# Optimization experiments

Measured on AMD Instinct MI355X. Metric: run time of the kernel, lower is better.

Reference implementation:

```python
import jax, jax.numpy as jnp
import numpy as np

D_MODEL = 768
NUM_HEADS = 12
HEAD_DIM = D_MODEL // NUM_HEADS
BATCH = 1
SEQ = 4096


def setup_inputs() -> dict:
    key = jax.random.key(0)
    ks = jax.random.split(key, 11)
    s = 0.02
    return {
        "q": jax.random.normal(ks[0], (BATCH, SEQ, D_MODEL), jnp.float32),
        "k": jax.random.normal(ks[1], (BATCH, SEQ, D_MODEL), jnp.float32),
        "v": jax.random.normal(ks[2], (BATCH, SEQ, D_MODEL), jnp.float32),
        "Wq": jax.random.normal(ks[3], (D_MODEL, D_MODEL), jnp.float32) * s,
        "bq": jnp.zeros((D_MODEL,), jnp.float32),
        "Wk": jax.random.normal(ks[4], (D_MODEL, D_MODEL), jnp.float32) * s,
        "bk": jnp.zeros((D_MODEL,), jnp.float32),
        "Wv": jax.random.normal(ks[5], (D_MODEL, D_MODEL), jnp.float32) * s,
        "bv": jnp.zeros((D_MODEL,), jnp.float32),
        "Wo": jax.random.normal(ks[6], (D_MODEL, D_MODEL), jnp.float32) * s,
        "bo": jnp.zeros((D_MODEL,), jnp.float32),
    }


def reference(q, k, v, Wq, bq, Wk, bk, Wv, bv, Wo, bo):
    B, S, D = q.shape
    H, Hd = NUM_HEADS, HEAD_DIM
    # linear projections (torch Linear: x @ W.T + b)
    qh = (q @ Wq.T + bq).reshape(B, S, H, Hd).transpose(0, 2, 1, 3)  # [B,H,S,Hd]
    kh = (k @ Wk.T + bk).reshape(B, S, H, Hd).transpose(0, 2, 1, 3)
    vh = (v @ Wv.T + bv).reshape(B, S, H, Hd).transpose(0, 2, 1, 3)
    scale = 1.0 / jnp.sqrt(jnp.asarray(Hd, qh.dtype))
    scores = jnp.einsum("bhsd,bhtd->bhst", qh, kh) * scale  # [B,H,S,S]
    weights = jax.nn.softmax(scores, axis=-1)
    attn = jnp.einsum("bhst,bhtd->bhsd", weights, vh)  # [B,H,S,Hd]
    attn = attn.transpose(0, 2, 1, 3).reshape(B, S, D)
    return attn @ Wo.T + bo
```

## Files before the change

### kernel.cpp

```cpp
#include <hip/hip_runtime.h>

#define S_LEN 4096
#define DMODEL 768
#define NHEAD 12
#define HD 64

typedef __bf16 bf16x8 __attribute__((ext_vector_type(8)));
typedef __bf16 bf16x4 __attribute__((ext_vector_type(4)));
typedef float f32x4 __attribute__((ext_vector_type(4)));
typedef float f32x16 __attribute__((ext_vector_type(16)));
typedef unsigned short u16x8 __attribute__((ext_vector_type(8)));
typedef unsigned short u16x4 __attribute__((ext_vector_type(4)));
typedef _Float16 f16x4 __attribute__((ext_vector_type(4)));

#if __has_builtin(__builtin_amdgcn_exp2f)
#define EXP2F(x) __builtin_amdgcn_exp2f(x)
#else
#define EXP2F(x) exp2f(x)
#endif

#define MFMA32(a, b, c) __builtin_amdgcn_mfma_f32_32x32x16_bf16(a, b, c, 0, 0, 0)

__device__ __forceinline__ unsigned short f2bf(float f) {
  unsigned int u = __float_as_uint(f);
  u += 0x7fffu + ((u >> 16) & 1u);
  return (unsigned short)(u >> 16);
}

__device__ __forceinline__ void gload_lds16(const void* g, void* l) {
  __builtin_amdgcn_global_load_lds(
      (__attribute__((address_space(1))) void*)g,
      (__attribute__((address_space(3))) void*)l, 16, 0, 0);
}

struct CvtArgs {
  const float* src[7];
  unsigned short* dst[7];
  int n[7];
};

__global__ __launch_bounds__(256) void cvt_kernel(CvtArgs a) {
  const int seg = blockIdx.y;
  const int n = a.n[seg];
  const int i = (blockIdx.x * 256 + threadIdx.x) * 8;
  if (i >= n) return;
  const float* s = a.src[seg] + i;
  u16x8 o;
#pragma unroll
  for (int j = 0; j < 8; ++j) o[j] = f2bf(s[j]);
  *reinterpret_cast<u16x8*>(a.dst[seg] + i) = o;
}

struct QkvArgs {
  const unsigned short* A[3];
  const unsigned short* W[3];
  const float* bias[3];
  unsigned short* dst[3];
  float scale[3];
};

__global__ __launch_bounds__(256) void qkv_gemm(QkvArgs a) {
  __shared__ unsigned char lds[32768];
  const int z = blockIdx.z;
  const unsigned short* __restrict__ A = a.A[z];
  const unsigned short* __restrict__ B = a.W[z];
  const float* __restrict__ bias = a.bias[z];
  unsigned short* __restrict__ dst = a.dst[z];
  const float scale = a.scale[z];

  const int tid = threadIdx.x;
  const int lane = tid & 63;
  const int w = tid >> 6;
  const int wr = w >> 1, wc = w & 1;
  const int c = lane & 15, g = lane >> 4;
  const int m0 = blockIdx.x * 128;
  const int n0 = blockIdx.y * 128;

  f32x4 acc[4][4] = {};

  for (int kt = 0; kt < DMODEL / 64; ++kt) {
#pragma unroll
    for (int p = 0; p < 4; ++p) {
      const int te = p * 256 + tid;
      const int row = te >> 3;
      const int sb = ((te & 7) * 16) ^ ((row & 7) << 4);
      gload_lds16(A + (size_t)(m0 + row) * DMODEL + kt * 64 + (sb >> 1), &lds[te * 16]);
      gload_lds16(B + (size_t)(n0 + row) * DMODEL + kt * 64 + (sb >> 1), &lds[16384 + te * 16]);
    }
    __syncthreads();

    bf16x8 af[4][2], bfr[4][2];
#pragma unroll
    for (int mb = 0; mb < 4; ++mb)
#pragma unroll
      for (int ks = 0; ks < 2; ++ks) {
        const int row = wr * 64 + mb * 16 + c;
        const int byte = (ks * 64 + g * 16) ^ ((row & 7) << 4);
        af[mb][ks] = *reinterpret_cast<const bf16x8*>(&lds[row * 128 + byte]);
      }
#pragma unroll
    for (int nb = 0; nb < 4; ++nb)
#pragma unroll
      for (int ks = 0; ks < 2; ++ks) {
        const int row = wc * 64 + nb * 16 + c;
        const int byte = (ks * 64 + g * 16) ^ ((row & 7) << 4);
        bfr[nb][ks] = *reinterpret_cast<const bf16x8*>(&lds[16384 + row * 128 + byte]);
      }
    __builtin_amdgcn_s_setprio(1);
#pragma unroll
    for (int ks = 0; ks < 2; ++ks)
#pragma unroll
      for (int mb = 0; mb < 4; ++mb)
#pragma unroll
        for (int nb = 0; nb < 4; ++nb)
          acc[mb][nb] = __builtin_amdgcn_mfma_f32_16x16x32_bf16(
              af[mb][ks], bfr[nb][ks], acc[mb][nb], 0, 0, 0);
    __builtin_amdgcn_s_setprio(0);
    __syncthreads();
  }

#pragma unroll
  for (int mb = 0; mb < 4; ++mb) {
#pragma unroll
    for (int nb = 0; nb < 4; ++nb) {
      const int n = n0 + wc * 64 + nb * 16 + c;
      const float bv = bias[n];
#pragma unroll
      for (int r = 0; r < 4; ++r) {
        const int m = m0 + wr * 64 + mb * 16 + g * 4 + r;
        const float v = (acc[mb][nb][r] + bv) * scale;
        const int hh = n >> 6, hd = n & 63;
        if (z != 2) {
          dst[((size_t)hh * S_LEN + m) * HD + hd] = f2bf(v);
        } else {
          const int mp = (m & ~12) | ((m & 4) << 1) | ((m & 8) >> 1);
          dst[((size_t)hh * HD + hd) * S_LEN + mp] = f2bf(v);
        }
      }
    }
  }
}

__global__ __launch_bounds__(256) void gemm_out(
    const unsigned short* __restrict__ A, const unsigned short* __restrict__ B,
    const float* __restrict__ bias, float* __restrict__ dst) {
  __shared__ unsigned char lds[32768];
  const int tid = threadIdx.x;
  const int lane = tid & 63;
  const int w = tid >> 6;
  const int wr = w >> 1, wc = w & 1;
  const int c = lane & 15, g = lane >> 4;
  const int m0 = blockIdx.x * 128;
  const int n0 = blockIdx.y * 128;

  f32x4 acc[4][4] = {};

  for (int kt = 0; kt < DMODEL / 64; ++kt) {
#pragma unroll
    for (int p = 0; p < 4; ++p) {
      const int te = p * 256 + tid;
      const int row = te >> 3;
      const int sb = ((te & 7) * 16) ^ ((row & 7) << 4);
      gload_lds16(A + (size_t)(m0 + row) * DMODEL + kt * 64 + (sb >> 1), &lds[te * 16]);
      gload_lds16(B + (size_t)(n0 + row) * DMODEL + kt * 64 + (sb >> 1), &lds[16384 + te * 16]);
    }
    __syncthreads();

    bf16x8 af[4][2], bfr[4][2];
#pragma unroll
    for (int mb = 0; mb < 4; ++mb)
#pragma unroll
      for (int ks = 0; ks < 2; ++ks) {
        const int row = wr * 64 + mb * 16 + c;
        const int byte = (ks * 64 + g * 16) ^ ((row & 7) << 4);
        af[mb][ks] = *reinterpret_cast<const bf16x8*>(&lds[row * 128 + byte]);
      }
#pragma unroll
    for (int nb = 0; nb < 4; ++nb)
#pragma unroll
      for (int ks = 0; ks < 2; ++ks) {
        const int row = wc * 64 + nb * 16 + c;
        const int byte = (ks * 64 + g * 16) ^ ((row & 7) << 4);
        bfr[nb][ks] = *reinterpret_cast<const bf16x8*>(&lds[16384 + row * 128 + byte]);
      }
    __builtin_amdgcn_s_setprio(1);
#pragma unroll
    for (int ks = 0; ks < 2; ++ks)
#pragma unroll
      for (int mb = 0; mb < 4; ++mb)
#pragma unroll
        for (int nb = 0; nb < 4; ++nb)
          acc[mb][nb] = __builtin_amdgcn_mfma_f32_16x16x32_bf16(
              af[mb][ks], bfr[nb][ks], acc[mb][nb], 0, 0, 0);
    __builtin_amdgcn_s_setprio(0);
    __syncthreads();
  }

#pragma unroll
  for (int mb = 0; mb < 4; ++mb)
#pragma unroll
    for (int nb = 0; nb < 4; ++nb) {
      const int n = n0 + wc * 64 + nb * 16 + c;
      const float bv = bias[n];
#pragma unroll
      for (int r = 0; r < 4; ++r) {
        const int m = m0 + wr * 64 + mb * 16 + g * 4 + r;
        dst[(size_t)m * DMODEL + n] = acc[mb][nb][r] + bv;
      }
    }
}

__global__ __launch_bounds__(256) void attn_kernel(
    const unsigned short* __restrict__ qh,
    const unsigned short* __restrict__ kh,
    const unsigned short* __restrict__ vtp,
    _Float16* __restrict__ pacc,
    float* __restrict__ prs) {
  __shared__ unsigned char lds[49152];
  const int tid = threadIdx.x;
  const int lane = tid & 63;
  const int w = tid >> 6;
  const int c5 = lane & 31;
  const int h2 = lane >> 5;
  const int hh = blockIdx.y;
  const int split = blockIdx.z;
  const int qw = blockIdx.x * 128 + w * 32;
  const int kv0 = split * (S_LEN / 2);
  const int NKT = (S_LEN / 2) / 64;

  bf16x8 qa[4];
#pragma unroll
  for (int ks = 0; ks < 4; ++ks)
    qa[ks] = *reinterpret_cast<const bf16x8*>(
        qh + ((size_t)hh * S_LEN + qw + c5) * HD + ks * 16 + h2 * 8);

  const int r63 = tid & 63;
  const unsigned short* ksrc =
      kh + ((size_t)hh * S_LEN + kv0 + r63) * HD + (tid >> 6) * 8;
  const unsigned short* vsrc =
      vtp + ((size_t)hh * HD + r63) * S_LEN + kv0 + (tid >> 6) * 8;
  const int dL = tid * 16;

  auto stage = [&](int bo) {
    gload_lds16(ksrc, &lds[bo + dL]);
    gload_lds16(ksrc + 32, &lds[bo + 4096 + dL]);
    gload_lds16(vsrc, &lds[bo + 8192 + dL]);
    gload_lds16(vsrc + 32, &lds[bo + 12288 + dL]);
    ksrc += 64 * HD;
    vsrc += 64;
  };

  stage(0);
  stage(16384);

  f32x16 accO[2] = {};
  float rs0 = 0.f, rs1 = 0.f, rs2 = 0.f, rs3 = 0.f;

  auto compute = [&](const unsigned char* Kb, const unsigned char* Vb) {
    f32x16 s0 = {}, s1 = {};
    __builtin_amdgcn_s_setprio(1);
#pragma unroll
    for (int ks = 0; ks < 4; ++ks) {
      const unsigned char* kbase = Kb + (ks * 2 + h2) * 1024 + c5 * 16;
      const bf16x8 k0 = *reinterpret_cast<const bf16x8*>(kbase);
      const bf16x8 k1 = *reinterpret_cast<const bf16x8*>(kbase + 512);
      s0 = MFMA32(k0, qa[ks], s0);
      s1 = MFMA32(k1, qa[ks], s1);
    }
    __builtin_amdgcn_s_setprio(0);

#pragma unroll
    for (int t = 0; t < 2; ++t)
#pragma unroll
      for (int ss = 0; ss < 2; ++ss) {
        const unsigned char* vbase = Vb + (t * 4 + ss * 2 + h2) * 1024 + c5 * 16;
        const bf16x8 va0 = *reinterpret_cast<const bf16x8*>(vbase);
        const bf16x8 va1 = *reinterpret_cast<const bf16x8*>(vbase + 512);
        bf16x8 pb;
        float racc = 0.f;
#pragma unroll
        for (int r = 0; r < 8; ++r) {
          const float e = EXP2F(t ? s1[ss * 8 + r] : s0[ss * 8 + r]);
          racc += e;
          pb[r] = (__bf16)e;
        }
        if (t == 0) { if (ss == 0) rs0 += racc; else rs1 += racc; }
        else        { if (ss == 0) rs2 += racc; else rs3 += racc; }
        __builtin_amdgcn_s_setprio(1);
        accO[0] = MFMA32(va0, pb, accO[0]);
        accO[1] = MFMA32(va1, pb, accO[1]);
        __builtin_amdgcn_s_setprio(0);
      }
  };

  int boC = 0;
  int boS = 32768;
  for (int t = 0; t < NKT; ++t) {
    if (t + 2 < NKT) {
      asm volatile("s_waitcnt vmcnt(4)" ::: "memory");
      __builtin_amdgcn_sched_barrier(0);
      __builtin_amdgcn_s_barrier();
      __builtin_amdgcn_sched_barrier(0);
      stage(boS);
    } else if (t + 1 < NKT) {
      asm volatile("s_waitcnt vmcnt(4)" ::: "memory");
      __builtin_amdgcn_sched_barrier(0);
      __builtin_amdgcn_s_barrier();
      __builtin_amdgcn_sched_barrier(0);
    } else {
      asm volatile("s_waitcnt vmcnt(0)" ::: "memory");
      __builtin_amdgcn_sched_barrier(0);
      __builtin_amdgcn_s_barrier();
      __builtin_amdgcn_sched_barrier(0);
    }
    compute(&lds[boC], &lds[boC + 8192]);
    boC += 16384; if (boC == 49152) boC = 0;
    boS += 16384; if (boS == 49152) boS = 0;
  }

  float rsA = (rs0 + rs1) + (rs2 + rs3);
  rsA += __shfl_xor(rsA, 32);
  const size_t hqbase = ((size_t)split * NHEAD + hh) * S_LEN + qw + c5;
  if (h2 == 0) prs[hqbase] = rsA * 0.015625f;
#pragma unroll
  for (int dt = 0; dt < 2; ++dt)
#pragma unroll
    for (int rr = 0; rr < 4; ++rr) {
      f16x4 o;
#pragma unroll
      for (int j = 0; j < 4; ++j)
        o[j] = (_Float16)(accO[dt][rr * 4 + j] * 0.015625f);
      *reinterpret_cast<f16x4*>(
          pacc + hqbase * 64 + dt * 32 + rr * 8 + h2 * 4) = o;
    }
}

__global__ __launch_bounds__(256) void combine_kernel(
    const _Float16* __restrict__ pacc, const float* __restrict__ prs,
    unsigned short* __restrict__ attb) {
  const int idx = blockIdx.x * 256 + threadIdx.x;
  const int hq = idx >> 4;
  const int d4 = (idx & 15) * 4;
  const int h = hq >> 12;
  const int q = hq & 4095;
  const size_t o0 = (size_t)hq * 64 + d4;
  const size_t o1 = o0 + (size_t)NHEAD * S_LEN * 64;
  const f16x4 av = *reinterpret_cast<const f16x4*>(pacc + o0);
  const f16x4 bv = *reinterpret_cast<const f16x4*>(pacc + o1);
  const float inv = 1.f / (prs[hq] + prs[hq + NHEAD * S_LEN]);
  u16x4 ov;
#pragma unroll
  for (int j = 0; j < 4; ++j)
    ov[j] = f2bf(((float)av[j] + (float)bv[j]) * inv);
  *reinterpret_cast<u16x4*>(attb + (size_t)q * DMODEL + h * HD + d4) = ov;
}

extern "C" void kernel_launch(void* const* d_in, const int* in_sizes, int n_in,
                              void* d_out, int out_size, void* d_ws, size_t ws_size,
                              hipStream_t stream) {
  (void)in_sizes; (void)n_in; (void)out_size;
  const float* q  = (const float*)d_in[0];
  const float* k  = (const float*)d_in[1];
  const float* v  = (const float*)d_in[2];
  const float* Wq = (const float*)d_in[3];
  const float* bq = (const float*)d_in[4];
  const float* Wk = (const float*)d_in[5];
  const float* bk = (const float*)d_in[6];
  const float* Wv = (const float*)d_in[7];
  const float* bv = (const float*)d_in[8];
  const float* Wo = (const float*)d_in[9];
  const float* bo = (const float*)d_in[10];
  float* out = (float*)d_out;

  const size_t SD = (size_t)S_LEN * DMODEL;
  const size_t DD = (size_t)DMODEL * DMODEL;
  if (ws_size < (7 * SD + 4 * DD) * 2) return;

  unsigned short* ws   = (unsigned short*)d_ws;
  unsigned short* qbf  = ws;
  unsigned short* kbf  = qbf + SD;
  unsigned short* vbf  = kbf + SD;
  unsigned short* wqb  = vbf + SD;
  unsigned short* wkb  = wqb + DD;
  unsigned short* wvb  = wkb + DD;
  unsigned short* wob  = wvb + DD;
  unsigned short* qhb  = wob + DD;
  unsigned short* khb  = qhb + SD;
  unsigned short* vtb  = khb + SD;
  unsigned short* attb = vtb + SD;

  _Float16* pacc = (_Float16*)qbf;
  float*    prs  = (float*)wqb;

  CvtArgs ca;
  ca.src[0] = q;  ca.dst[0] = qbf; ca.n[0] = (int)SD;
  ca.src[1] = k;  ca.dst[1] = kbf; ca.n[1] = (int)SD;
  ca.src[2] = v;  ca.dst[2] = vbf; ca.n[2] = (int)SD;
  ca.src[3] = Wq; ca.dst[3] = wqb; ca.n[3] = (int)DD;
  ca.src[4] = Wk; ca.dst[4] = wkb; ca.n[4] = (int)DD;
  ca.src[5] = Wv; ca.dst[5] = wvb; ca.n[5] = (int)DD;
  ca.src[6] = Wo; ca.dst[6] = wob; ca.n[6] = (int)DD;
  cvt_kernel<<<dim3(1536, 7), 256, 0, stream>>>(ca);

  QkvArgs qa;
  qa.A[0] = qbf; qa.W[0] = wqb; qa.bias[0] = bq; qa.dst[0] = qhb;
  qa.scale[0] = 0.18033688011112042f;
  qa.A[1] = kbf; qa.W[1] = wkb; qa.bias[1] = bk; qa.dst[1] = khb;
  qa.scale[1] = 1.0f;
  qa.A[2] = vbf; qa.W[2] = wvb; qa.bias[2] = bv; qa.dst[2] = vtb;
  qa.scale[2] = 1.0f;
  qkv_gemm<<<dim3(32, 6, 3), 256, 0, stream>>>(qa);

  attn_kernel<<<dim3(S_LEN / 128, NHEAD, 2), 256, 0, stream>>>(
      qhb, khb, vtb, pacc, prs);

  combine_kernel<<<dim3((NHEAD * S_LEN * 16) / 256), 256, 0, stream>>>(
      pacc, prs, attb);

  gemm_out<<<dim3(32, 6), 256, 0, stream>>>(attb, wob, bo, out);
}
```

Baseline: 127.5 us.

## Fuse fp32 activation conversion into QKV GEMM and split attention KV three ways

The QKV GEMM now loads fp32 activations directly into LDS and converts them to bf16 while building MFMA fragments, so the separate conversion pass over q/k/v and its bf16 staging buffers go away. Only the weights are still converted up front. The attention kernel's KV range is split three ways instead of two, raising the block count for better CU occupancy, and the combine kernel merges three partials. In exchange the GEMM stages twice the bytes for A in LDS and does conversion work per tile, and combine reads more partial data.

```diff
diff --git a/kernel.cpp b/kernel.cpp
--- a/kernel.cpp
+++ b/kernel.cpp
@@ -34,16 +34,13 @@
 }
 
 struct CvtArgs {
-  const float* src[7];
-  unsigned short* dst[7];
-  int n[7];
+  const float* src[4];
+  unsigned short* dst[4];
 };
 
 __global__ __launch_bounds__(256) void cvt_kernel(CvtArgs a) {
   const int seg = blockIdx.y;
-  const int n = a.n[seg];
   const int i = (blockIdx.x * 256 + threadIdx.x) * 8;
-  if (i >= n) return;
   const float* s = a.src[seg] + i;
   u16x8 o;
 #pragma unroll
@@ -52,7 +49,7 @@
 }
 
 struct QkvArgs {
-  const unsigned short* A[3];
+  const float* A[3];
   const unsigned short* W[3];
   const float* bias[3];
   unsigned short* dst[3];
@@ -60,9 +57,9 @@
 };
 
 __global__ __launch_bounds__(256) void qkv_gemm(QkvArgs a) {
-  __shared__ unsigned char lds[32768];
+  __shared__ unsigned char lds[49152];
   const int z = blockIdx.z;
-  const unsigned short* __restrict__ A = a.A[z];
+  const float* __restrict__ A = a.A[z];
   const unsigned short* __restrict__ B = a.W[z];
   const float* __restrict__ bias = a.bias[z];
   unsigned short* __restrict__ dst = a.dst[z];
@@ -80,12 +77,19 @@
 
   for (int kt = 0; kt < DMODEL / 64; ++kt) {
 #pragma unroll
+    for (int p = 0; p < 8; ++p) {
+      const int te = p * 256 + tid;
+      const int row = te >> 4;
+      const int fidx = ((te & 15) * 4) ^ ((row & 7) << 2);
+      gload_lds16(A + (size_t)(m0 + row) * DMODEL + kt * 64 + fidx, &lds[te * 16]);
+    }
+#pragma unroll
     for (int p = 0; p < 4; ++p) {
       const int te = p * 256 + tid;
       const int row = te >> 3;
       const int sb = ((te & 7) * 16) ^ ((row & 7) << 4);
-      gload_lds16(A + (size_t)(m0 + row) * DMODEL + kt * 64 + (sb >> 1), &lds[te * 16]);
-      gload_lds16(B + (size_t)(n0 + row) * DMODEL + kt * 64 + (sb >> 1), &lds[16384 + te * 16]);
+      gload_lds16(B + (size_t)(n0 + row) * DMODEL + kt * 64 + (sb >> 1),
+                  &lds[32768 + te * 16]);
     }
     __syncthreads();
 
@@ -95,8 +99,14 @@
 #pragma unroll
       for (int ks = 0; ks < 2; ++ks) {
         const int row = wr * 64 + mb * 16 + c;
-        const int byte = (ks * 64 + g * 16) ^ ((row & 7) << 4);
-        af[mb][ks] = *reinterpret_cast<const bf16x8*>(&lds[row * 128 + byte]);
+        const int swz = (row & 7) << 4;
+        const int s0 = ks * 128 + g * 32;
+        const f32x4 lo = *reinterpret_cast<const f32x4*>(&lds[row * 256 + (s0 ^ swz)]);
+        const f32x4 hi = *reinterpret_cast<const f32x4*>(&lds[row * 256 + ((s0 + 16) ^ swz)]);
+        bf16x8 v;
+#pragma unroll
+        for (int i = 0; i < 4; ++i) { v[i] = (__bf16)lo[i]; v[4 + i] = (__bf16)hi[i]; }
+        af[mb][ks] = v;
       }
 #pragma unroll
     for (int nb = 0; nb < 4; ++nb)
@@ -104,7 +114,7 @@
       for (int ks = 0; ks < 2; ++ks) {
         const int row = wc * 64 + nb * 16 + c;
         const int byte = (ks * 64 + g * 16) ^ ((row & 7) << 4);
-        bfr[nb][ks] = *reinterpret_cast<const bf16x8*>(&lds[16384 + row * 128 + byte]);
+        bfr[nb][ks] = *reinterpret_cast<const bf16x8*>(&lds[32768 + row * 128 + byte]);
       }
     __builtin_amdgcn_s_setprio(1);
 #pragma unroll
@@ -225,8 +235,9 @@
   const int hh = blockIdx.y;
   const int split = blockIdx.z;
   const int qw = blockIdx.x * 128 + w * 32;
-  const int kv0 = split * (S_LEN / 2);
-  const int NKT = (S_LEN / 2) / 64;
+  const int kt0 = (64 * split) / 3;
+  const int nkt = (64 * (split + 1)) / 3 - kt0;
+  const int kv0 = kt0 * 64;
 
   bf16x8 qa[4];
 #pragma unroll
@@ -295,14 +306,14 @@
 
   int boC = 0;
   int boS = 32768;
-  for (int t = 0; t < NKT; ++t) {
-    if (t + 2 < NKT) {
+  for (int t = 0; t < nkt; ++t) {
+    if (t + 2 < nkt) {
       asm volatile("s_waitcnt vmcnt(4)" ::: "memory");
       __builtin_amdgcn_sched_barrier(0);
       __builtin_amdgcn_s_barrier();
       __builtin_amdgcn_sched_barrier(0);
       stage(boS);
-    } else if (t + 1 < NKT) {
+    } else if (t + 1 < nkt) {
       asm volatile("s_waitcnt vmcnt(4)" ::: "memory");
       __builtin_amdgcn_sched_barrier(0);
       __builtin_amdgcn_s_barrier();
@@ -343,15 +354,16 @@
   const int d4 = (idx & 15) * 4;
   const int h = hq >> 12;
   const int q = hq & 4095;
+  const int HS = NHEAD * S_LEN;
   const size_t o0 = (size_t)hq * 64 + d4;
-  const size_t o1 = o0 + (size_t)NHEAD * S_LEN * 64;
-  const f16x4 av = *reinterpret_cast<const f16x4*>(pacc + o0);
-  const f16x4 bv = *reinterpret_cast<const f16x4*>(pacc + o1);
-  const float inv = 1.f / (prs[hq] + prs[hq + NHEAD * S_LEN]);
+  const f16x4 a0 = *reinterpret_cast<const f16x4*>(pacc + o0);
+  const f16x4 a1 = *reinterpret_cast<const f16x4*>(pacc + o0 + (size_t)HS * 64);
+  const f16x4 a2 = *reinterpret_cast<const f16x4*>(pacc + o0 + (size_t)2 * HS * 64);
+  const float inv = 1.f / (prs[hq] + prs[hq + HS] + prs[hq + 2 * HS]);
   u16x4 ov;
 #pragma unroll
   for (int j = 0; j < 4; ++j)
-    ov[j] = f2bf(((float)av[j] + (float)bv[j]) * inv);
+    ov[j] = f2bf(((float)a0[j] + (float)a1[j] + (float)a2[j]) * inv);
   *reinterpret_cast<u16x4*>(attb + (size_t)q * DMODEL + h * HD + d4) = ov;
 }
 
@@ -377,41 +389,34 @@
   if (ws_size < (7 * SD + 4 * DD) * 2) return;
 
   unsigned short* ws   = (unsigned short*)d_ws;
-  unsigned short* qbf  = ws;
-  unsigned short* kbf  = qbf + SD;
-  unsigned short* vbf  = kbf + SD;
-  unsigned short* wqb  = vbf + SD;
-  unsigned short* wkb  = wqb + DD;
-  unsigned short* wvb  = wkb + DD;
-  unsigned short* wob  = wvb + DD;
-  unsigned short* qhb  = wob + DD;
-  unsigned short* khb  = qhb + SD;
-  unsigned short* vtb  = khb + SD;
-  unsigned short* attb = vtb + SD;
-
-  _Float16* pacc = (_Float16*)qbf;
-  float*    prs  = (float*)wqb;
+  unsigned short* wqb  = ws;
+  unsigned short* wkb  = ws + DD;
+  unsigned short* wvb  = ws + 2 * DD;
+  unsigned short* qhb  = ws + 3 * SD;
+  unsigned short* khb  = ws + 4 * SD;
+  unsigned short* vtb  = ws + 5 * SD;
+  unsigned short* attb = ws + 6 * SD;
+  float*          prs  = (float*)(ws + 7 * SD);
+  unsigned short* wob  = ws + 7 * SD + 294912;
+  _Float16*       pacc = (_Float16*)ws;
 
   CvtArgs ca;
-  ca.src[0] = q;  ca.dst[0] = qbf; ca.n[0] = (int)SD;
-  ca.src[1] = k;  ca.dst[1] = kbf; ca.n[1] = (int)SD;
-  ca.src[2] = v;  ca.dst[2] = vbf; ca.n[2] = (int)SD;
-  ca.src[3] = Wq; ca.dst[3] = wqb; ca.n[3] = (int)DD;
-  ca.src[4] = Wk; ca.dst[4] = wkb; ca.n[4] = (int)DD;
-  ca.src[5] = Wv; ca.dst[5] = wvb; ca.n[5] = (int)DD;
-  ca.src[6] = Wo; ca.dst[6] = wob; ca.n[6] = (int)DD;
-  cvt_kernel<<<dim3(1536, 7), 256, 0, stream>>>(ca);
+  ca.src[0] = Wq; ca.dst[0] = wqb;
+  ca.src[1] = Wk; ca.dst[1] = wkb;
+  ca.src[2] = Wv; ca.dst[2] = wvb;
+  ca.src[3] = Wo; ca.dst[3] = wob;
+  cvt_kernel<<<dim3(288, 4), 256, 0, stream>>>(ca);
 
   QkvArgs qa;
-  qa.A[0] = qbf; qa.W[0] = wqb; qa.bias[0] = bq; qa.dst[0] = qhb;
+  qa.A[0] = q; qa.W[0] = wqb; qa.bias[0] = bq; qa.dst[0] = qhb;
   qa.scale[0] = 0.18033688011112042f;
-  qa.A[1] = kbf; qa.W[1] = wkb; qa.bias[1] = bk; qa.dst[1] = khb;
+  qa.A[1] = k; qa.W[1] = wkb; qa.bias[1] = bk; qa.dst[1] = khb;
   qa.scale[1] = 1.0f;
-  qa.A[2] = vbf; qa.W[2] = wvb; qa.bias[2] = bv; qa.dst[2] = vtb;
+  qa.A[2] = v; qa.W[2] = wvb; qa.bias[2] = bv; qa.dst[2] = vtb;
   qa.scale[2] = 1.0f;
   qkv_gemm<<<dim3(32, 6, 3), 256, 0, stream>>>(qa);
 
-  attn_kernel<<<dim3(S_LEN / 128, NHEAD, 2), 256, 0, stream>>>(
+  attn_kernel<<<dim3(S_LEN / 128, NHEAD, 3), 256, 0, stream>>>(
       qhb, khb, vtb, pacc, prs);
 
   combine_kernel<<<dim3((NHEAD * S_LEN * 16) / 256), 256, 0, stream>>>(
```

Result: slower. 148.8 us (+16.6%).

## Split attention KV into four chunks with 512-thread blocks

Applied to the files above, without the earlier changes.

The attention kernel now runs 512-thread blocks covering 256 queries each and splits the key/value sequence four ways instead of two. With twice as many threads, each thread issues half as many LDS staging loads per tile. The combine kernel sums four partial outputs and row sums, and the workspace layout is rearranged so the larger partial buffers fit. This aims to raise parallelism and occupancy, at the cost of more partial-result traffic in the combine step and a workspace layout that is trickier to keep correct.

```diff
diff --git a/kernel.cpp b/kernel.cpp
--- a/kernel.cpp
+++ b/kernel.cpp
@@ -210,7 +210,7 @@
     }
 }
 
-__global__ __launch_bounds__(256) void attn_kernel(
+__global__ __launch_bounds__(512, 6) void attn_kernel(
     const unsigned short* __restrict__ qh,
     const unsigned short* __restrict__ kh,
     const unsigned short* __restrict__ vtp,
@@ -224,9 +224,9 @@
   const int h2 = lane >> 5;
   const int hh = blockIdx.y;
   const int split = blockIdx.z;
-  const int qw = blockIdx.x * 128 + w * 32;
-  const int kv0 = split * (S_LEN / 2);
-  const int NKT = (S_LEN / 2) / 64;
+  const int qw = blockIdx.x * 256 + w * 32;
+  const int kv0 = split * (S_LEN / 4);
+  const int nkt = (S_LEN / 4) / 64;
 
   bf16x8 qa[4];
 #pragma unroll
@@ -234,18 +234,15 @@
     qa[ks] = *reinterpret_cast<const bf16x8*>(
         qh + ((size_t)hh * S_LEN + qw + c5) * HD + ks * 16 + h2 * 8);
 
-  const int r63 = tid & 63;
   const unsigned short* ksrc =
-      kh + ((size_t)hh * S_LEN + kv0 + r63) * HD + (tid >> 6) * 8;
+      kh + ((size_t)hh * S_LEN + kv0 + (tid & 63)) * HD + (tid >> 6) * 8;
   const unsigned short* vsrc =
-      vtp + ((size_t)hh * HD + r63) * S_LEN + kv0 + (tid >> 6) * 8;
+      vtp + ((size_t)hh * HD + (tid & 63)) * S_LEN + kv0 + (tid >> 6) * 8;
   const int dL = tid * 16;
 
   auto stage = [&](int bo) {
     gload_lds16(ksrc, &lds[bo + dL]);
-    gload_lds16(ksrc + 32, &lds[bo + 4096 + dL]);
     gload_lds16(vsrc, &lds[bo + 8192 + dL]);
-    gload_lds16(vsrc + 32, &lds[bo + 12288 + dL]);
     ksrc += 64 * HD;
     vsrc += 64;
   };
@@ -295,15 +292,15 @@
 
   int boC = 0;
   int boS = 32768;
-  for (int t = 0; t < NKT; ++t) {
-    if (t + 2 < NKT) {
-      asm volatile("s_waitcnt vmcnt(4)" ::: "memory");
+  for (int t = 0; t < nkt; ++t) {
+    if (t + 2 < nkt) {
+      asm volatile("s_waitcnt vmcnt(2)" ::: "memory");
       __builtin_amdgcn_sched_barrier(0);
       __builtin_amdgcn_s_barrier();
       __builtin_amdgcn_sched_barrier(0);
       stage(boS);
-    } else if (t + 1 < NKT) {
-      asm volatile("s_waitcnt vmcnt(4)" ::: "memory");
+    } else if (t + 1 < nkt) {
+      asm volatile("s_waitcnt vmcnt(2)" ::: "memory");
       __builtin_amdgcn_sched_barrier(0);
       __builtin_amdgcn_s_barrier();
       __builtin_amdgcn_sched_barrier(0);
@@ -343,15 +340,21 @@
   const int d4 = (idx & 15) * 4;
   const int h = hq >> 12;
   const int q = hq & 4095;
+  const int HS = NHEAD * S_LEN;
   const size_t o0 = (size_t)hq * 64 + d4;
-  const size_t o1 = o0 + (size_t)NHEAD * S_LEN * 64;
-  const f16x4 av = *reinterpret_cast<const f16x4*>(pacc + o0);
-  const f16x4 bv = *reinterpret_cast<const f16x4*>(pacc + o1);
-  const float inv = 1.f / (prs[hq] + prs[hq + NHEAD * S_LEN]);
+  float acc4[4] = {0.f, 0.f, 0.f, 0.f};
+  float rs = 0.f;
+#pragma unroll
+  for (int k = 0; k < 4; ++k) {
+    const f16x4 av = *reinterpret_cast<const f16x4*>(pacc + o0 + (size_t)k * HS * 64);
+#pragma unroll
+    for (int j = 0; j < 4; ++j) acc4[j] += (float)av[j];
+    rs += prs[hq + k * HS];
+  }
+  const float inv = 1.f / rs;
   u16x4 ov;
 #pragma unroll
-  for (int j = 0; j < 4; ++j)
-    ov[j] = f2bf(((float)av[j] + (float)bv[j]) * inv);
+  for (int j = 0; j < 4; ++j) ov[j] = f2bf(acc4[j] * inv);
   *reinterpret_cast<u16x4*>(attb + (size_t)q * DMODEL + h * HD + d4) = ov;
 }
 
@@ -378,19 +381,18 @@
 
   unsigned short* ws   = (unsigned short*)d_ws;
   unsigned short* qbf  = ws;
-  unsigned short* kbf  = qbf + SD;
-  unsigned short* vbf  = kbf + SD;
-  unsigned short* wqb  = vbf + SD;
-  unsigned short* wkb  = wqb + DD;
-  unsigned short* wvb  = wkb + DD;
-  unsigned short* wob  = wvb + DD;
-  unsigned short* qhb  = wob + DD;
-  unsigned short* khb  = qhb + SD;
-  unsigned short* vtb  = khb + SD;
-  unsigned short* attb = vtb + SD;
-
-  _Float16* pacc = (_Float16*)qbf;
-  float*    prs  = (float*)wqb;
+  unsigned short* kbf  = ws + SD;
+  unsigned short* vbf  = ws + 2 * SD;
+  unsigned short* wqb  = ws + 3 * SD;
+  unsigned short* wkb  = ws + 3 * SD + DD;
+  unsigned short* wvb  = ws + 3 * SD + 2 * DD;
+  unsigned short* qhb  = ws + 4 * SD;
+  unsigned short* khb  = ws + 5 * SD;
+  unsigned short* vtb  = ws + 6 * SD;
+  float*          prs  = (float*)(ws + 7 * SD);
+  unsigned short* wob  = ws + 7 * SD + 393216;
+  _Float16*       pacc = (_Float16*)ws;
+  unsigned short* attb = ws + 4 * SD;
 
   CvtArgs ca;
   ca.src[0] = q;  ca.dst[0] = qbf; ca.n[0] = (int)SD;
@@ -411,7 +413,7 @@
   qa.scale[2] = 1.0f;
   qkv_gemm<<<dim3(32, 6, 3), 256, 0, stream>>>(qa);
 
-  attn_kernel<<<dim3(S_LEN / 128, NHEAD, 2), 256, 0, stream>>>(
+  attn_kernel<<<dim3(S_LEN / 256, NHEAD, 4), 512, 0, stream>>>(
       qhb, khb, vtb, pacc, prs);
 
   combine_kernel<<<dim3((NHEAD * S_LEN * 16) / 256), 256, 0, stream>>>(
```

After: 383.0 us. +200.3%, slower.
